# Kernel tuning notes

Measured on AMD Instinct MI355X. Metric: run time of the kernel, lower is better.

## Reference

```python
import jax, jax.numpy as jnp
import numpy as np

NUM_EMBEDDINGS = 1000
EMBEDDING_DIM = 64
COMMITMENT_COST = 10.0


def setup_inputs() -> dict:
    key = jax.random.key(0)
    k1, k2 = jax.random.split(key)
    x = jax.random.normal(k1, (16, EMBEDDING_DIM, 2048), dtype=jnp.float32)  # [B, D, L]
    emb_w = jax.random.normal(k2, (NUM_EMBEDDINGS, EMBEDDING_DIM), dtype=jnp.float32)
    return {"x": x, "emb_w": emb_w}


def reference(x, emb_w):
    # [B, D, L] -> [B, L, D]
    inputs = jnp.transpose(x, (0, 2, 1))
    B, L, D = inputs.shape
    K = emb_w.shape[0]
    flat = inputs.reshape(-1, D)  # [N, D]

    # squared L2 distances to every codebook vector: [N, K]
    distances = (
        jnp.sum(flat * flat, axis=1, keepdims=True)
        + jnp.sum(emb_w * emb_w, axis=1)
        - 2.0 * jnp.matmul(flat, emb_w.T)
    )
    idx = jnp.argmin(distances, axis=1)  # [N]

    # direct gather instead of one-hot matmul (same math)
    quantized = emb_w[idx].reshape(B, L, D)

    e_latent_loss = jnp.mean((jax.lax.stop_gradient(quantized) - inputs) ** 2)
    q_latent_loss = jnp.mean((quantized - jax.lax.stop_gradient(inputs)) ** 2)
    loss = q_latent_loss + COMMITMENT_COST * e_latent_loss

    # straight-through estimator
    quantized_st = inputs + jax.lax.stop_gradient(quantized - inputs)

    counts = jnp.zeros((K,), dtype=jnp.int32).at[idx].add(1)
    embedding_usage = jnp.sum(counts > 0)

    out = jnp.transpose(quantized_st, (0, 2, 1))  # back to [B, D, L]
    return out, loss, embedding_usage, idx[:, None]
```

## Files before the change

kernel.cpp:

```cpp
#include <hip/hip_runtime.h>

using v4f = float __attribute__((ext_vector_type(4)));

constexpr int NTOK = 32768;
constexpr int DIMS = 64;
constexpr int KCODES = 1000;
constexpr int NSPLIT = 8;
constexpr int CPSPLIT = 128;
constexpr float BIG = 3.4e38f;

__global__ __launch_bounds__(256, 4) void vq_main(
    const float* __restrict__ x, const float* __restrict__ emb,
    float* __restrict__ pval, int* __restrict__ pidx,
    float* __restrict__ loss_accum, int* __restrict__ usage)
{
    __shared__ float ns[CPSPLIT];

    const int tid   = threadIdx.x;
    const int split = blockIdx.x >> 7;
    const int tb    = blockIdx.x & 127;
    const int token = tb * 256 + tid;
    const int b     = token >> 11;
    const int l     = token & 2047;
    const float* xp = x + ((size_t)b << 17) + l;
    const int cbase = split * CPSPLIT;

    if (blockIdx.x == 0) {
        for (int u = tid; u < KCODES; u += 256) usage[u] = 0;
        if (tid == 0) *loss_accum = 0.f;
    }

    if (tid < CPSPLIT) {
        int g = cbase + tid;
        float nv = BIG;
        if (g < KCODES) {
            const float* e = emb + (size_t)g * DIMS;
            float sq[4];
            #pragma unroll
            for (int q = 0; q < 4; ++q) {
                float s = 0.f;
                #pragma unroll
                for (int i = 0; i < 4; ++i) {
                    v4f v = *reinterpret_cast<const v4f*>(e + q * 16 + i * 4);
                    s = fmaf(v[0], v[0], fmaf(v[1], v[1], fmaf(v[2], v[2], fmaf(v[3], v[3], s))));
                }
                sq[q] = s;
            }
            nv = (sq[0] + sq[1]) + (sq[2] + sq[3]);
        }
        ns[tid] = nv;
    }

    float xv[DIMS];
    #pragma unroll
    for (int d = 0; d < DIMS; ++d) xv[d] = xp[(size_t)d * 2048];
    #pragma unroll
    for (int d = 0; d < DIMS; ++d) asm volatile("" : "+v"(xv[d]));

    __syncthreads();

    float minv = BIG;
    int   mini = 0;

    for (int g4 = 0; g4 < CPSPLIT / 4; ++g4) {
        const int c0 = cbase + g4 * 4;
        if (c0 >= KCODES) break;
        const float* eg = emb + (size_t)c0 * DIMS;
        float acc[4] = {0.f, 0.f, 0.f, 0.f};
        #pragma unroll
        for (int d4 = 0; d4 < 16; ++d4) {
            #pragma unroll
            for (int c = 0; c < 4; ++c) {
                v4f ev = *reinterpret_cast<const v4f*>(eg + c * DIMS + d4 * 4);
                #pragma unroll
                for (int k = 0; k < 4; ++k)
                    acc[c] = fmaf(xv[d4 * 4 + k], ev[k], acc[c]);
            }
        }
        #pragma unroll
        for (int c = 0; c < 4; ++c) {
            float dist = fmaf(-2.f, acc[c], ns[g4 * 4 + c]);
            if (dist < minv) { minv = dist; mini = c0 + c; }
        }
    }

    pval[split * NTOK + token] = minv;
    pidx[split * NTOK + token] = mini;
}

__global__ __launch_bounds__(256) void vq_output(
    const float* __restrict__ x, const float* __restrict__ emb,
    const float* __restrict__ pval, const int* __restrict__ pidx,
    float* __restrict__ out, float* __restrict__ idx_f,
    float* __restrict__ loss_accum, int* __restrict__ usage)
{
    const int tid   = threadIdx.x;
    const int ll    = tid & 63;
    const int dg    = tid >> 6;
    const int token = blockIdx.x * 64 + ll;

    float bv = pval[token];
    int   bi = pidx[token];
    #pragma unroll
    for (int s = 1; s < NSPLIT; ++s) {
        float v  = pval[s * NTOK + token];
        int   i2 = pidx[s * NTOK + token];
        if (v < bv) { bv = v; bi = i2; }
    }
    if (dg == 0) {
        idx_f[token] = (float)bi;
        atomicOr(&usage[bi], 1);
    }

    const int b = token >> 11, l = token & 2047;
    const float* xb = x   + ((size_t)b << 17) + l + (size_t)(dg * 16) * 2048;
    float*       ob = out + ((size_t)b << 17) + l + (size_t)(dg * 16) * 2048;
    const float* e  = emb + (size_t)bi * DIMS + dg * 16;

    float lsum = 0.f;
    #pragma unroll
    for (int q4 = 0; q4 < 4; ++q4) {
        v4f q = *reinterpret_cast<const v4f*>(e + q4 * 4);
        #pragma unroll
        for (int k = 0; k < 4; ++k) {
            const int d = q4 * 4 + k;
            float xvv  = xb[(size_t)d * 2048];
            float diff = q[k] - xvv;
            lsum = fmaf(diff, diff, lsum);
            ob[(size_t)d * 2048] = xvv + diff;
        }
    }

    #pragma unroll
    for (int off = 32; off >= 1; off >>= 1) lsum += __shfl_xor(lsum, off);
    __shared__ float bsum[4];
    if ((tid & 63) == 0) bsum[tid >> 6] = lsum;
    __syncthreads();
    if (tid == 0) atomicAdd(loss_accum, bsum[0] + bsum[1] + bsum[2] + bsum[3]);
}

__global__ void vq_finalize(const float* __restrict__ loss_accum, const int* __restrict__ usage,
                            float* __restrict__ o_scalars)
{
    __shared__ int wsum[16];
    int tid = threadIdx.x;
    int c = (tid < KCODES && usage[tid]) ? 1 : 0;
    #pragma unroll
    for (int off = 32; off >= 1; off >>= 1) c += __shfl_xor(c, off);
    if ((tid & 63) == 0) wsum[tid >> 6] = c;
    __syncthreads();
    if (tid == 0) {
        int total = 0;
        #pragma unroll
        for (int i = 0; i < 16; ++i) total += wsum[i];
        float m = *loss_accum / 2097152.0f;
        o_scalars[0] = 11.0f * m;
        o_scalars[1] = (float)total;
    }
}

extern "C" void kernel_launch(void* const* d_in, const int* in_sizes, int n_in,
                              void* d_out, int out_size, void* d_ws, size_t ws_size,
                              hipStream_t stream)
{
    const float* x   = (const float*)d_in[0];
    const float* emb = (const float*)d_in[1];

    float* o       = (float*)d_out;
    float* out     = o;
    float* o_scal  = o + 2097152;
    float* o_idx   = o + 2097154;

    char*  ws         = (char*)d_ws;
    float* loss_accum = (float*)(ws);
    int*   usage      = (int*)(ws + 64);
    float* pval       = (float*)(ws + 8192);
    int*   pidx       = (int*)(ws + 8192 + NSPLIT * NTOK * sizeof(float));

    vq_main<<<NSPLIT * 128, 256, 0, stream>>>(x, emb, pval, pidx, loss_accum, usage);
    vq_output<<<NTOK / 64, 256, 0, stream>>>(x, emb, pval, pidx, out, o_idx, loss_accum, usage);
    vq_finalize<<<1, 1024, 0, stream>>>(loss_accum, usage, o_scal);
}
```

Before: 167.2 us.

## Stage token vectors in swizzled LDS and widen codebook groups per pass

Each thread's 64-dim token vector now goes into shared memory with an XOR swizzle, replacing the 64 registers that held it. Each pass now computes dot products against 10 codes instead of 4. The split count changes from 8×128 to 4×250 codes so the groups divide evenly and no bounds check is needed. The aim is to reuse each x load across more codes and cut register pressure, at the cost of 64KB of LDS per block, extra LDS reads and lower occupancy (launch bounds 2).

```diff
diff --git a/kernel.cpp b/kernel.cpp
--- a/kernel.cpp
+++ b/kernel.cpp
@@ -5,85 +5,101 @@
 constexpr int NTOK = 32768;
 constexpr int DIMS = 64;
 constexpr int KCODES = 1000;
-constexpr int NSPLIT = 8;
-constexpr int CPSPLIT = 128;
+constexpr int NSPLIT = 4;
+constexpr int CPSPLIT = 250;
+constexpr int GRP = 10;
 constexpr float BIG = 3.4e38f;
 
-__global__ __launch_bounds__(256, 4) void vq_main(
+__global__ __launch_bounds__(256, 2) void vq_main(
     const float* __restrict__ x, const float* __restrict__ emb,
     float* __restrict__ pval, int* __restrict__ pidx,
     float* __restrict__ loss_accum, int* __restrict__ usage)
 {
+    __shared__ float xs[256 * DIMS];
     __shared__ float ns[CPSPLIT];
 
     const int tid   = threadIdx.x;
     const int split = blockIdx.x >> 7;
-    const int tb    = blockIdx.x & 127;
-    const int token = tb * 256 + tid;
-    const int b     = token >> 11;
-    const int l     = token & 2047;
-    const float* xp = x + ((size_t)b << 17) + l;
+    const int tblk  = blockIdx.x & 127;
+    const int tok0  = tblk * 256;
+    const int b     = tok0 >> 11;
+    const int l0    = tok0 & 2047;
     const int cbase = split * CPSPLIT;
+    const float* xgb = x + ((size_t)b << 17) + l0;
 
     if (blockIdx.x == 0) {
         for (int u = tid; u < KCODES; u += 256) usage[u] = 0;
         if (tid == 0) *loss_accum = 0.f;
     }
 
-    if (tid < CPSPLIT) {
-        int g = cbase + tid;
-        float nv = BIG;
-        if (g < KCODES) {
-            const float* e = emb + (size_t)g * DIMS;
-            float sq[4];
+    {
+        const int sw = (tid & 7) << 2;
+        #pragma unroll
+        for (int d4 = 0; d4 < 16; ++d4) {
+            v4f v;
             #pragma unroll
-            for (int q = 0; q < 4; ++q) {
-                float s = 0.f;
-                #pragma unroll
-                for (int i = 0; i < 4; ++i) {
-                    v4f v = *reinterpret_cast<const v4f*>(e + q * 16 + i * 4);
-                    s = fmaf(v[0], v[0], fmaf(v[1], v[1], fmaf(v[2], v[2], fmaf(v[3], v[3], s))));
-                }
-                sq[q] = s;
-            }
-            nv = (sq[0] + sq[1]) + (sq[2] + sq[3]);
+            for (int k = 0; k < 4; ++k) v[k] = xgb[(size_t)(d4 * 4 + k) * 2048 + tid];
+            *reinterpret_cast<v4f*>(&xs[tid * DIMS + ((d4 * 4) ^ sw)]) = v;
         }
-        ns[tid] = nv;
     }
 
-    float xv[DIMS];
-    #pragma unroll
-    for (int d = 0; d < DIMS; ++d) xv[d] = xp[(size_t)d * 2048];
-    #pragma unroll
-    for (int d = 0; d < DIMS; ++d) asm volatile("" : "+v"(xv[d]));
+    if (tid < CPSPLIT) {
+        const float* e = emb + (size_t)(cbase + tid) * DIMS;
+        float sq[4];
+        #pragma unroll
+        for (int q = 0; q < 4; ++q) {
+            float s = 0.f;
+            #pragma unroll
+            for (int i = 0; i < 4; ++i) {
+                v4f v = *reinterpret_cast<const v4f*>(e + q * 16 + i * 4);
+                s = fmaf(v[0], v[0], fmaf(v[1], v[1], fmaf(v[2], v[2], fmaf(v[3], v[3], s))));
+            }
+            sq[q] = s;
+        }
+        ns[tid] = (sq[0] + sq[1]) + (sq[2] + sq[3]);
+    }
 
     __syncthreads();
+
+    const float* xptr[16];
+    {
+        const int sw = (tid & 7) << 2;
+        #pragma unroll
+        for (int d4 = 0; d4 < 16; ++d4)
+            xptr[d4] = &xs[tid * DIMS + ((d4 * 4) ^ sw)];
+    }
 
     float minv = BIG;
     int   mini = 0;
 
-    for (int g4 = 0; g4 < CPSPLIT / 4; ++g4) {
-        const int c0 = cbase + g4 * 4;
-        if (c0 >= KCODES) break;
+    for (int g = 0; g < CPSPLIT / GRP; ++g) {
+        const int c0 = cbase + g * GRP;
         const float* eg = emb + (size_t)c0 * DIMS;
-        float acc[4] = {0.f, 0.f, 0.f, 0.f};
+
+        float acc[GRP];
+        #pragma unroll
+        for (int c = 0; c < GRP; ++c) acc[c] = 0.f;
+
         #pragma unroll
         for (int d4 = 0; d4 < 16; ++d4) {
+            v4f xq = *reinterpret_cast<const v4f*>(xptr[d4]);
             #pragma unroll
-            for (int c = 0; c < 4; ++c) {
+            for (int c = 0; c < GRP; ++c) {
                 v4f ev = *reinterpret_cast<const v4f*>(eg + c * DIMS + d4 * 4);
                 #pragma unroll
                 for (int k = 0; k < 4; ++k)
-                    acc[c] = fmaf(xv[d4 * 4 + k], ev[k], acc[c]);
+                    acc[c] = fmaf(xq[k], ev[k], acc[c]);
             }
         }
+
         #pragma unroll
-        for (int c = 0; c < 4; ++c) {
-            float dist = fmaf(-2.f, acc[c], ns[g4 * 4 + c]);
+        for (int c = 0; c < GRP; ++c) {
+            float dist = fmaf(-2.f, acc[c], ns[g * GRP + c]);
             if (dist < minv) { minv = dist; mini = c0 + c; }
         }
     }
 
+    const int token = tok0 + tid;
     pval[split * NTOK + token] = minv;
     pidx[split * NTOK + token] = mini;
 }
```

New measurement: 170.5 us. 1.02x slower.
